# Kernel tuning notes

Hardware: AMD Instinct MI355X
Metric: run time of the kernel (lower is better)

## Reference

```python
import jax, jax.numpy as jnp
import numpy as np

# Static config (Phi-3-medium style)
HIDDEN = 5120
N_HEADS = 40
N_KV_HEADS = 10
HEAD_DIM = 128  # padded == original here
ROPE_THETA = 10000.0
B, S = 8, 1024  # 8 packed sequences of length 1024 -> T = 8192
T = B * S


def apply_rope(x, pos, theta=ROPE_THETA):
    # x: [T, N, H], pos: [T]  (neox-style split-half rotary over full head dim)
    H = x.shape[-1]
    half = H // 2
    inv_freq = 1.0 / (theta ** (jnp.arange(half, dtype=jnp.float32) * 2.0 / H))
    ang = pos.astype(jnp.float32)[:, None] * inv_freq  # [T, half]
    cos = jnp.cos(ang)[:, None, :]  # [T, 1, half]
    sin = jnp.sin(ang)[:, None, :]
    x1, x2 = x[..., :half], x[..., half:]
    return jnp.concatenate([x1 * cos - x2 * sin, x2 * cos + x1 * sin], axis=-1).astype(x.dtype)


def setup_inputs() -> dict:
    key = jax.random.key(0)
    k1, k2, k3 = jax.random.split(key, 3)
    x = jax.random.normal(k1, (T, HIDDEN), dtype=jnp.float32)
    w_qkv = jax.random.normal(k2, (HIDDEN, N_HEADS + 2 * N_KV_HEADS, HEAD_DIM), dtype=jnp.float32) * (HIDDEN ** -0.5)
    w_o = jax.random.normal(k3, (N_HEADS, HEAD_DIM, HIDDEN), dtype=jnp.float32) * ((N_HEADS * HEAD_DIM) ** -0.5)
    positions = jnp.tile(jnp.arange(S, dtype=jnp.int32), B)  # per-sequence positions
    return {"x": x, "w_qkv": w_qkv, "w_o": w_o, "positions": positions}


def reference(x, w_qkv, w_o, positions):
    # Fused QKV projection: [T, D] x [D, N_total, H] -> [T, N_total, H]
    qkv = jnp.einsum('td,dnh->tnh', x, w_qkv)
    q, k, v = jnp.split(qkv, [N_HEADS, N_HEADS + N_KV_HEADS], axis=1)
    q = apply_rope(q, positions)
    k = apply_rope(k, positions)

    # KV cache is simply the (rope'd) k/v written at token slots (no quantization).
    G = N_HEADS // N_KV_HEADS  # GQA group size
    qb = q.reshape(B, S, N_KV_HEADS, G, HEAD_DIM)
    kb = k.reshape(B, S, N_KV_HEADS, HEAD_DIM)
    vb = v.reshape(B, S, N_KV_HEADS, HEAD_DIM)

    scale = HEAD_DIM ** -0.5
    scores = jnp.einsum('bqkgh,bskh->bkgqs', qb, kb) * scale  # [B,K,G,S,S]
    causal = jnp.tril(jnp.ones((S, S), dtype=bool))
    scores = jnp.where(causal, scores, jnp.finfo(scores.dtype).min)
    probs = jax.nn.softmax(scores, axis=-1)
    out = jnp.einsum('bkgqs,bskh->bqkgh', probs, vb)  # [B,S,K,G,H]
    out = out.reshape(T, N_HEADS, HEAD_DIM)

    o = jnp.einsum('tnh,nhd->td', out, w_o)
    return o
```

## Files before the change

### kernel.cpp

```cpp
#include <hip/hip_runtime.h>
#include <hip/hip_bf16.h>

typedef unsigned short u16;
typedef __attribute__((ext_vector_type(8))) __bf16 bf16x8;
typedef __attribute__((ext_vector_type(4))) float f32x4;

#define GLDS16(gsrc, ldst)                                                         \
  __builtin_amdgcn_global_load_lds(                                               \
      (__attribute__((address_space(1))) const void*)(gsrc),                      \
      (__attribute__((address_space(3))) void*)(ldst), 16, 0, 0)

#define BAR() asm volatile("s_barrier" ::: "memory")
#define LG0()                                            \
  {                                                      \
    asm volatile("s_waitcnt lgkmcnt(0)" ::: "memory");   \
    __builtin_amdgcn_sched_barrier(0);                   \
  }
#define VMW2()                                           \
  {                                                      \
    asm volatile("s_waitcnt vmcnt(2)" ::: "memory");     \
    __builtin_amdgcn_sched_barrier(0);                   \
  }
#define VMW0()                                           \
  {                                                      \
    asm volatile("s_waitcnt vmcnt(0)" ::: "memory");     \
    __builtin_amdgcn_sched_barrier(0);                   \
  }

__device__ __forceinline__ float bf2f(u16 u) {
  union { unsigned int i; float f; } v; v.i = ((unsigned int)u) << 16; return v.f;
}
__device__ __forceinline__ u16 f2bf(float f) {
  union { float f; unsigned int i; } v; v.f = f;
  return (u16)((v.i + 0x7fffu + ((v.i >> 16) & 1u)) >> 16);
}

__global__ void cvt_x_kernel(const float4* __restrict__ in, ushort4* __restrict__ out) {
  size_t i = (size_t)blockIdx.x * 256 + threadIdx.x;
  float4 v = in[i];
  ushort4 o;
  o.x = f2bf(v.x); o.y = f2bf(v.y); o.z = f2bf(v.z); o.w = f2bf(v.w);
  out[i] = o;
}

__global__ void tconv_kernel(const float* __restrict__ in, u16* __restrict__ out,
                             int R, int C) {
  __shared__ float tile[64][65];
  const int c0 = blockIdx.x * 64, r0 = blockIdx.y * 64;
  const int tx = threadIdx.x & 63, ty = threadIdx.x >> 6;
#pragma unroll
  for (int p = 0; p < 16; ++p) {
    int row = p * 4 + ty;
    tile[row][tx] = in[(size_t)(r0 + row) * C + c0 + tx];
  }
  __syncthreads();
#pragma unroll
  for (int p = 0; p < 16; ++p) {
    int row = p * 4 + ty;
    out[(size_t)(c0 + row) * R + r0 + tx] = f2bf(tile[tx][row]);
  }
}

__device__ __forceinline__ void lda4(bf16x8 a[4][2], const u16* b0, const u16* b1) {
#pragma unroll
  for (int mt = 0; mt < 4; ++mt) {
    a[mt][0] = *(const bf16x8*)(b0 + mt * 1024);
    a[mt][1] = *(const bf16x8*)(b1 + mt * 1024);
  }
}
__device__ __forceinline__ void ldb2(bf16x8 b[2][2], const u16* b0, const u16* b1) {
#pragma unroll
  for (int nt = 0; nt < 2; ++nt) {
    b[nt][0] = *(const bf16x8*)(b0 + nt * 1024);
    b[nt][1] = *(const bf16x8*)(b1 + nt * 1024);
  }
}
template <int MH, int NH>
__device__ __forceinline__ void mma8(f32x4 acc[8][4], const bf16x8 a[4][2], const bf16x8 b[2][2]) {
  __builtin_amdgcn_s_setprio(1);
#pragma unroll
  for (int mt = 0; mt < 4; ++mt)
#pragma unroll
    for (int nt = 0; nt < 2; ++nt) {
      f32x4 c = acc[MH * 4 + mt][NH * 2 + nt];
      c = __builtin_amdgcn_mfma_f32_16x16x32_bf16(a[mt][0], b[nt][0], c, 0, 0, 0);
      c = __builtin_amdgcn_mfma_f32_16x16x32_bf16(a[mt][1], b[nt][1], c, 0, 0, 0);
      acc[MH * 4 + mt][NH * 2 + nt] = c;
    }
  __builtin_amdgcn_s_setprio(0);
}

__global__ __launch_bounds__(512, 2) void gemm_bt256_kernel(
    const u16* __restrict__ A, const u16* __restrict__ BT,
    float* __restrict__ Cf, u16* __restrict__ Cb, int M, int N, int K,
    int nbm, int nbn) {
  __shared__ __align__(16) u16 As_[2][16384];
  __shared__ __align__(16) u16 Bs_[2][16384];
  u16* As0 = &As_[0][0]; u16* As1 = &As_[1][0];
  u16* Bs0 = &Bs_[0][0]; u16* Bs1 = &Bs_[1][0];

  const int nwg = nbm * nbn;
  int wg = (int)blockIdx.x;
  wg = (wg & 7) * (nwg >> 3) + (wg >> 3);
  const int PW = 10;
  const int per_panel = PW * nbm;
  const int panel = wg / per_panel;
  const int rem = wg - panel * per_panel;
  const int pw = min(PW, nbn - panel * PW);
  const int bn = panel * PW + rem % pw;
  const int bm = rem / pw;
  const int m0 = bm * 256, n0 = bn * 256;

  const int tid = threadIdx.x;
  const int wave = tid >> 6, lane = tid & 63;
  const int quad = lane >> 4, l16 = lane & 15;
  const int wm = wave >> 2, wn = wave & 3;

  const int rl = lane >> 3;
  const int cs = ((lane & 7) ^ rl) * 8;
  const u16* pA = A + (size_t)(m0 + wave * 8 + rl) * K + cs;
  const u16* pB = BT + (size_t)(n0 + wave * 8 + rl) * K + cs;
  const size_t r64 = (size_t)64 * K, r128 = (size_t)128 * K;

#define STG(p, hofs, kt, lds)                                         \
  {                                                                   \
    GLDS16((p) + (hofs) + (size_t)(kt) * 64, (lds) + wave * 512);     \
    GLDS16((p) + (hofs) + r64 + (size_t)(kt) * 64, (lds) + 4096 + wave * 512); \
  }

  const int eo = l16 & 7;
  const int aoff0 = l16 * 64 + ((quad ^ eo) * 8);
  const int aoff1 = l16 * 64 + (((4 | quad) ^ eo) * 8);
  const u16* Ab0 = As0 + wm * 8192;
  const u16* Ab1 = As1 + wm * 8192;
  const u16* Bb0 = Bs0 + wn * 4096;
  const u16* Bb1 = Bs1 + wn * 4096;

  f32x4 acc[8][4] = {};
  bf16x8 a[4][2], b[2][2];

  const int NIT = K >> 7;

  STG(pA, 0, 0, As0);
  STG(pA, r128, 0, As0 + 8192);
  STG(pB, 0, 0, Bs0);
  STG(pB, r128, 0, Bs0 + 8192);
  STG(pA, 0, 1, As1);
  VMW2();
  BAR();

#pragma unroll 1
  for (int it = 0; it < NIT; ++it) {
    const int t = 2 * it;
    const bool sg = (it < NIT - 1);

    lda4(a, Ab0 + aoff0, Ab0 + aoff1);
    ldb2(b, Bb0 + aoff0, Bb0 + aoff1);
    STG(pA, r128, t + 1, As1 + 8192);
    BAR(); LG0();
    mma8<0, 0>(acc, a, b);
    BAR();
    ldb2(b, Bb0 + 2048 + aoff0, Bb0 + 2048 + aoff1);
    STG(pB, 0, t + 1, Bs1);
    BAR(); LG0();
    mma8<0, 1>(acc, a, b);
    BAR();
    lda4(a, Ab0 + 4096 + aoff0, Ab0 + 4096 + aoff1);
    STG(pB, r128, t + 1, Bs1 + 8192);
    BAR(); LG0();
    mma8<1, 1>(acc, a, b);
    BAR();
    ldb2(b, Bb0 + aoff0, Bb0 + aoff1);
    if (sg) STG(pA, 0, t + 2, As0);
    BAR(); LG0();
    mma8<1, 0>(acc, a, b);
    if (sg) { VMW2(); } else { VMW0(); }
    BAR();

    lda4(a, Ab1 + aoff0, Ab1 + aoff1);
    ldb2(b, Bb1 + aoff0, Bb1 + aoff1);
    if (sg) STG(pA, r128, t + 2, As0 + 8192);
    BAR(); LG0();
    mma8<0, 0>(acc, a, b);
    BAR();
    ldb2(b, Bb1 + 2048 + aoff0, Bb1 + 2048 + aoff1);
    if (sg) STG(pB, 0, t + 2, Bs0);
    BAR(); LG0();
    mma8<0, 1>(acc, a, b);
    BAR();
    lda4(a, Ab1 + 4096 + aoff0, Ab1 + 4096 + aoff1);
    if (sg) STG(pB, r128, t + 2, Bs0 + 8192);
    BAR(); LG0();
    mma8<1, 1>(acc, a, b);
    BAR();
    ldb2(b, Bb1 + aoff0, Bb1 + aoff1);
    if (sg) STG(pA, 0, t + 3, As1);
    BAR(); LG0();
    mma8<1, 0>(acc, a, b);
    if (sg) { VMW2(); } else { VMW0(); }
    BAR();
  }
#undef STG

  const int crow0 = m0 + wm * 128 + quad * 4;
  const int ccol0 = n0 + wn * 64 + l16;
#pragma unroll
  for (int mt = 0; mt < 8; ++mt)
#pragma unroll
    for (int nt = 0; nt < 4; ++nt)
#pragma unroll
      for (int r = 0; r < 4; ++r) {
        int row = crow0 + mt * 16 + r;
        int col = ccol0 + nt * 16;
        float v = acc[mt][nt][r];
        if (Cb) Cb[(size_t)row * N + col] = f2bf(v);
        else    Cf[(size_t)row * N + col] = v;
      }
}

__global__ void rope_kernel(u16* __restrict__ qkv, const int* __restrict__ positions) {
  int idx = blockIdx.x * 256 + threadIdx.x;
  int j = idx & 63, t = idx >> 6;
  float inv = exp2f(-(float)j * 0.20762050593046014f);
  float ang = (float)positions[t] * inv;
  float sn, cs;
  sincosf(ang, &sn, &cs);
  u16* row = qkv + (size_t)t * 7680;
#pragma unroll 2
  for (int h = 0; h < 50; ++h) {
    u16* p1 = row + h * 128 + j;
    float x1 = bf2f(p1[0]), x2 = bf2f(p1[64]);
    p1[0] = f2bf(x1 * cs - x2 * sn);
    p1[64] = f2bf(x2 * cs + x1 * sn);
  }
}

__global__ void vtrans_kernel(const u16* __restrict__ qkv, u16* __restrict__ vt) {
  __shared__ u16 tile[64][132];
  const int s0 = blockIdx.x * 64, kvh = blockIdx.y, b = blockIdx.z;
  const int tid = threadIdx.x;
#pragma unroll
  for (int p = 0; p < 8; ++p) {
    int sl = p * 8 + (tid >> 5);
    int d = (tid & 31) * 4;
    const u16* src = qkv + (size_t)(b * 1024 + s0 + sl) * 7680 + (50 + kvh) * 128 + d;
    ushort4 v = *(const ushort4*)src;
    tile[sl][d] = v.x; tile[sl][d + 1] = v.y; tile[sl][d + 2] = v.z; tile[sl][d + 3] = v.w;
  }
  __syncthreads();
#pragma unroll
  for (int p = 0; p < 8; ++p) {
    int d = p * 16 + (tid >> 4);
    int sl = (tid & 15) * 4;
    ushort4 v;
    v.x = tile[sl][d]; v.y = tile[sl + 1][d]; v.z = tile[sl + 2][d]; v.w = tile[sl + 3][d];
    u16* dst = vt + ((size_t)((b * 10 + kvh) * 128) + d) * 1024 + s0 + sl;
    *(ushort4*)dst = v;
  }
}

__global__ __launch_bounds__(256, 2) void attn_kernel(
    const u16* __restrict__ qkv, const u16* __restrict__ vt, u16* __restrict__ ao) {
  __shared__ __align__(16) u16 Ks[4][2048];
  __shared__ __align__(16) u16 VTs[2][4096];
  __shared__ __align__(16) u16 Ps[4][2][1024];

  const int tid = threadIdx.x, wave = tid >> 6, lane = tid & 63;
  const int quad = lane >> 4, l16 = lane & 15;
  const int q0 = blockIdx.x * 128, h = blockIdx.y, b = blockIdx.z;
  const int kvh = h >> 2;
  const float SCALE = 0.08838834764831845f;

  bf16x8 qf[2][4];
#pragma unroll
  for (int mt = 0; mt < 2; ++mt) {
    int t = b * 1024 + q0 + wave * 32 + mt * 16 + l16;
    const u16* qrow = qkv + (size_t)t * 7680 + h * 128;
#pragma unroll
    for (int ks = 0; ks < 4; ++ks)
      qf[mt][ks] = *(const bf16x8*)(qrow + ks * 32 + quad * 8);
  }

  f32x4 oa[2][8] = {};
  float mstate[2][4], lstate[2][4];
#pragma unroll
  for (int mt = 0; mt < 2; ++mt)
#pragma unroll
    for (int r = 0; r < 4; ++r) { mstate[mt][r] = -1e30f; lstate[mt][r] = 0.f; }

  const u16* Kbase = qkv + (size_t)(b * 1024) * 7680 + (40 + kvh) * 128;
  const u16* VTbase = vt + (size_t)((b * 10 + kvh) * 128) * 1024;

  const int nsteps = q0 / 64 + 2;
  for (int step = 0; step < nsteps; ++step) {
    const int s0 = step * 64;
    __syncthreads();
#pragma unroll
    for (int j = 0; j < 4; ++j) {
      int c = 4 * wave + j;
      int ksub = c >> 2, rg = c & 3;
      GLDS16(Kbase + (size_t)(s0 + rg * 16 + (lane >> 2)) * 7680 + ksub * 32 + (lane & 3) * 8,
             &Ks[ksub][rg * 512]);
      int vsub = c >> 3, dg = c & 7;
      GLDS16(VTbase + (size_t)(dg * 16 + (lane >> 2)) * 1024 + s0 + vsub * 32 + (lane & 3) * 8,
             &VTs[vsub][dg * 512]);
    }
    __syncthreads();

    f32x4 sa[2][4] = {};
#pragma unroll
    for (int ks = 0; ks < 4; ++ks) {
      bf16x8 kb[4];
#pragma unroll
      for (int nt = 0; nt < 4; ++nt)
        kb[nt] = *(const bf16x8*)&Ks[ks][(nt * 16 + l16) * 32 + quad * 8];
#pragma unroll
      for (int mt = 0; mt < 2; ++mt)
#pragma unroll
        for (int nt = 0; nt < 4; ++nt)
          sa[mt][nt] = __builtin_amdgcn_mfma_f32_16x16x32_bf16(qf[mt][ks], kb[nt], sa[mt][nt], 0, 0, 0);
    }

#pragma unroll
    for (int mt = 0; mt < 2; ++mt) {
#pragma unroll
      for (int r = 0; r < 4; ++r) {
        int qg = q0 + wave * 32 + mt * 16 + quad * 4 + r;
        float pv[4];
        float rowmax = -1e30f;
#pragma unroll
        for (int nt = 0; nt < 4; ++nt) {
          int sg = s0 + nt * 16 + l16;
          float v = sa[mt][nt][r] * SCALE;
          if (sg > qg) v = -1e30f;
          pv[nt] = v;
          rowmax = fmaxf(rowmax, v);
        }
#pragma unroll
        for (int off = 1; off < 16; off <<= 1)
          rowmax = fmaxf(rowmax, __shfl_xor(rowmax, off));
        float mnew = fmaxf(mstate[mt][r], rowmax);
        float alpha = __expf(mstate[mt][r] - mnew);
        mstate[mt][r] = mnew;
        float rs = 0.f;
#pragma unroll
        for (int nt = 0; nt < 4; ++nt) {
          float p = __expf(pv[nt] - mnew);
          rs += p;
          Ps[wave][nt >> 1][(mt * 16 + quad * 4 + r) * 32 + (nt & 1) * 16 + l16] = f2bf(p);
        }
#pragma unroll
        for (int off = 1; off < 16; off <<= 1)
          rs += __shfl_xor(rs, off);
        lstate[mt][r] = lstate[mt][r] * alpha + rs;
#pragma unroll
        for (int ntd = 0; ntd < 8; ++ntd) oa[mt][ntd][r] *= alpha;
      }
    }
    __syncthreads();

#pragma unroll
    for (int ks2 = 0; ks2 < 2; ++ks2) {
      bf16x8 pf[2];
#pragma unroll
      for (int mt = 0; mt < 2; ++mt)
        pf[mt] = *(const bf16x8*)&Ps[wave][ks2][(mt * 16 + l16) * 32 + quad * 8];
#pragma unroll
      for (int ntd = 0; ntd < 8; ++ntd) {
        bf16x8 vf = *(const bf16x8*)&VTs[ks2][(ntd * 16 + l16) * 32 + quad * 8];
#pragma unroll
        for (int mt = 0; mt < 2; ++mt)
          oa[mt][ntd] = __builtin_amdgcn_mfma_f32_16x16x32_bf16(pf[mt], vf, oa[mt][ntd], 0, 0, 0);
      }
    }
  }

#pragma unroll
  for (int mt = 0; mt < 2; ++mt)
#pragma unroll
    for (int ntd = 0; ntd < 8; ++ntd)
#pragma unroll
      for (int r = 0; r < 4; ++r) {
        int t = b * 1024 + q0 + wave * 32 + mt * 16 + quad * 4 + r;
        int d = ntd * 16 + l16;
        float v = oa[mt][ntd][r] / lstate[mt][r];
        ao[((size_t)t * 40 + h) * 128 + d] = f2bf(v);
      }
}

extern "C" void kernel_launch(void* const* d_in, const int* in_sizes, int n_in,
                              void* d_out, int out_size, void* d_ws, size_t ws_size,
                              hipStream_t stream) {
  const float* x = (const float*)d_in[0];
  const float* wqkv = (const float*)d_in[1];
  const float* wo = (const float*)d_in[2];
  const int* pos = (const int*)d_in[3];
  float* out = (float*)d_out;

  char* ws = (char*)d_ws;
  u16* xb = (u16*)(ws);
  u16* wT = (u16*)(ws + 83886080);
  u16* qkvb = (u16*)(ws + 83886080 + 78643200);
  u16* vt = (u16*)(ws + 83886080 + 78643200 + 125829120);

  cvt_x_kernel<<<40960, 256, 0, stream>>>((const float4*)x, (ushort4*)xb);
  tconv_kernel<<<dim3(120, 80), 256, 0, stream>>>(wqkv, wT, 5120, 7680);
  gemm_bt256_kernel<<<32 * 30, 512, 0, stream>>>(xb, wT, nullptr, qkvb, 8192, 7680, 5120, 32, 30);
  rope_kernel<<<2048, 256, 0, stream>>>(qkvb, pos);
  vtrans_kernel<<<dim3(16, 10, 8), 256, 0, stream>>>(qkvb, vt);
  tconv_kernel<<<dim3(80, 80), 256, 0, stream>>>(wo, wT, 5120, 5120);
  attn_kernel<<<dim3(8, 40, 8), 256, 0, stream>>>(qkvb, vt, xb);
  gemm_bt256_kernel<<<32 * 20, 512, 0, stream>>>(xb, wT, out, nullptr, 8192, 5120, 5120, 32, 20);
}
```

Baseline: 1.967 ms.

## Software-pipeline GEMM main loop with double-buffered registers and partial waitcnts

Rewrites the GEMM K-loop so LDS fragment reads for the next sub-tile are issued before the current MFMA block, using separate A/B register sets and partial lgkmcnt waits instead of full waits. It cuts the barriers per K tile from eight to two and reorders global-to-LDS staging so B tiles are prefetched one step further ahead. The aim is to hide LDS read latency behind MFMA and reduce barrier stalls, at the cost of more VGPRs and finely tuned wait counts that could race if they are wrong.

New measurement: 1.933 ms. Within noise of the previous version (-1.7%).

```diff
diff --git a/kernel.cpp b/kernel.cpp
--- a/kernel.cpp
+++ b/kernel.cpp
@@ -11,20 +11,15 @@
       (__attribute__((address_space(3))) void*)(ldst), 16, 0, 0)
 
 #define BAR() asm volatile("s_barrier" ::: "memory")
-#define LG0()                                            \
-  {                                                      \
-    asm volatile("s_waitcnt lgkmcnt(0)" ::: "memory");   \
-    __builtin_amdgcn_sched_barrier(0);                   \
-  }
-#define VMW2()                                           \
-  {                                                      \
-    asm volatile("s_waitcnt vmcnt(2)" ::: "memory");     \
-    __builtin_amdgcn_sched_barrier(0);                   \
-  }
-#define VMW0()                                           \
-  {                                                      \
-    asm volatile("s_waitcnt vmcnt(0)" ::: "memory");     \
-    __builtin_amdgcn_sched_barrier(0);                   \
+#define LGK(N)                                                      \
+  {                                                                 \
+    asm volatile("s_waitcnt lgkmcnt(" #N ")" ::: "memory");         \
+    __builtin_amdgcn_sched_barrier(0);                              \
+  }
+#define VMW(N)                                                      \
+  {                                                                 \
+    asm volatile("s_waitcnt vmcnt(" #N ")" ::: "memory");           \
+    __builtin_amdgcn_sched_barrier(0);                              \
   }
 
 __device__ __forceinline__ float bf2f(u16 u) {
@@ -137,69 +132,62 @@
   const u16* Bb1 = Bs1 + wn * 4096;
 
   f32x4 acc[8][4] = {};
-  bf16x8 a[4][2], b[2][2];
-
-  const int NIT = K >> 7;
+  bf16x8 a0[4][2], a1[4][2], bx[2][2], by[2][2];
+
+  const int NT = K >> 6;
 
   STG(pA, 0, 0, As0);
   STG(pA, r128, 0, As0 + 8192);
   STG(pB, 0, 0, Bs0);
   STG(pB, r128, 0, Bs0 + 8192);
+  STG(pB, 0, 1, Bs1);
+  STG(pB, r128, 1, Bs1 + 8192);
   STG(pA, 0, 1, As1);
-  VMW2();
+  VMW(6);
   BAR();
+  lda4(a0, Ab0 + aoff0, Ab0 + aoff1);
+  ldb2(bx, Bb0 + aoff0, Bb0 + aoff1);
+  __builtin_amdgcn_sched_barrier(0);
+
+#define TILE(t, AbR, BbR, AbN, BbN, AsN, AsR, BsR, B0r, B1r)                   \
+  {                                                                            \
+    const bool sg1 = (t) + 1 < NT, sg2 = (t) + 2 < NT;                         \
+                                                                       \
+    if (sg1) STG(pA, r128, (t) + 1, (AsN) + 8192);                             \
+    ldb2(B1r, (BbR) + 2048 + aoff0, (BbR) + 2048 + aoff1);                     \
+    LGK(4);                                                                    \
+    mma8<0, 0>(acc, a0, B0r);                                                  \
+                                                                       \
+    lda4(a1, (AbR) + 4096 + aoff0, (AbR) + 4096 + aoff1);                      \
+    LGK(8);                                                                    \
+    mma8<0, 1>(acc, a0, B1r);                                                  \
+    BAR();                                                                     \
+                                                                       \
+    if (sg2) STG(pB, 0, (t) + 2, (BsR));                                       \
+    LGK(0);                                                                    \
+    mma8<1, 1>(acc, a1, B1r);                                                  \
+    if (sg2) { VMW(2); } else { VMW(0); }                                      \
+    BAR();                                                                     \
+                                                                       \
+    if (sg1) {                                                                 \
+      lda4(a0, (AbN) + aoff0, (AbN) + aoff1);                                  \
+      ldb2(B1r, (BbN) + aoff0, (BbN) + aoff1);                                 \
+    }                                                                          \
+    if (sg2) {                                                                 \
+      STG(pB, r128, (t) + 2, (BsR) + 8192);                                    \
+      STG(pA, 0, (t) + 2, (AsR));                                              \
+    }                                                                          \
+    __builtin_amdgcn_sched_barrier(0);                                         \
+    mma8<1, 0>(acc, a1, B0r);                                                  \
+  }
 
 #pragma unroll 1
-  for (int it = 0; it < NIT; ++it) {
+  for (int it = 0; it < (NT >> 1); ++it) {
     const int t = 2 * it;
-    const bool sg = (it < NIT - 1);
-
-    lda4(a, Ab0 + aoff0, Ab0 + aoff1);
-    ldb2(b, Bb0 + aoff0, Bb0 + aoff1);
-    STG(pA, r128, t + 1, As1 + 8192);
-    BAR(); LG0();
-    mma8<0, 0>(acc, a, b);
-    BAR();
-    ldb2(b, Bb0 + 2048 + aoff0, Bb0 + 2048 + aoff1);
-    STG(pB, 0, t + 1, Bs1);
-    BAR(); LG0();
-    mma8<0, 1>(acc, a, b);
-    BAR();
-    lda4(a, Ab0 + 4096 + aoff0, Ab0 + 4096 + aoff1);
-    STG(pB, r128, t + 1, Bs1 + 8192);
-    BAR(); LG0();
-    mma8<1, 1>(acc, a, b);
-    BAR();
-    ldb2(b, Bb0 + aoff0, Bb0 + aoff1);
-    if (sg) STG(pA, 0, t + 2, As0);
-    BAR(); LG0();
-    mma8<1, 0>(acc, a, b);
-    if (sg) { VMW2(); } else { VMW0(); }
-    BAR();
-
-    lda4(a, Ab1 + aoff0, Ab1 + aoff1);
-    ldb2(b, Bb1 + aoff0, Bb1 + aoff1);
-    if (sg) STG(pA, r128, t + 2, As0 + 8192);
-    BAR(); LG0();
-    mma8<0, 0>(acc, a, b);
-    BAR();
-    ldb2(b, Bb1 + 2048 + aoff0, Bb1 + 2048 + aoff1);
-    if (sg) STG(pB, 0, t + 2, Bs0);
-    BAR(); LG0();
-    mma8<0, 1>(acc, a, b);
-    BAR();
-    lda4(a, Ab1 + 4096 + aoff0, Ab1 + 4096 + aoff1);
-    if (sg) STG(pB, r128, t + 2, Bs0 + 8192);
-    BAR(); LG0();
-    mma8<1, 1>(acc, a, b);
-    BAR();
-    ldb2(b, Bb1 + aoff0, Bb1 + aoff1);
-    if (sg) STG(pA, 0, t + 3, As1);
-    BAR(); LG0();
-    mma8<1, 0>(acc, a, b);
-    if (sg) { VMW2(); } else { VMW0(); }
-    BAR();
-  }
+    TILE(t, Ab0, Bb0, Ab1, Bb1, As1, As0, Bs0, bx, by);
+    TILE(t + 1, Ab1, Bb1, Ab0, Bb0, As0, As1, Bs1, by, bx);
+  }
+#undef TILE
 #undef STG
 
   const int crow0 = m0 + wm * 128 + quad * 4;
```
